# Kernel tuning notes

Hardware: AMD Instinct MI355X
Metric: run time of the kernel (lower is better)

The kernel has to match this reference:

```python
import jax, jax.numpy as jnp
import numpy as np

d_model = 512


def setup_inputs() -> dict:
    key = jax.random.key(0)
    k1, k2, k3, k4 = jax.random.split(key, 4)
    B, T, d_k = 8, 2048, 64
    scale = 1.0 / np.sqrt(d_model)
    x = jax.random.normal(k1, (B, T, d_model), dtype=jnp.float32)
    Wk = jax.random.normal(k2, (d_model, d_k), dtype=jnp.float32) * scale
    Wq = jax.random.normal(k3, (d_model, d_k), dtype=jnp.float32) * scale
    Wv = jax.random.normal(k4, (d_model, d_k), dtype=jnp.float32) * scale
    return {"x": x, "Wk": Wk, "Wq": Wq, "Wv": Wv}


def reference(x, Wk, Wq, Wv):
    # x: [B,T,C]; W*: [C,d_k]  (torch Linear weight is [d_k,C]; we store transposed)
    k = jnp.einsum('btc,cd->btd', x, Wk)
    q = jnp.einsum('btc,cd->btd', x, Wq)
    v = jnp.einsum('btc,cd->btd', x, Wv)
    d_k = k.shape[-1]
    scores = jnp.einsum('bqd,bkd->bqk', q, k) / jnp.sqrt(jnp.float32(d_k))
    attn = jax.nn.softmax(scores, axis=-1)  # [B,T,T]
    return jnp.einsum('bqk,bkd->bqd', attn, v)
```

## Files before the change

### kernel.cpp

```cpp
#include <hip/hip_runtime.h>
#include <hip/hip_bf16.h>
#include <stdint.h>


typedef short bf16x8 __attribute__((ext_vector_type(8)));
typedef float f32x4 __attribute__((ext_vector_type(4)));

#define MFMA_BF16 __builtin_amdgcn_mfma_f32_16x16x32_bf16

#define CEXP 0.18033688011112042f

__device__ __forceinline__ unsigned int pk2(float a, float b) {
    __hip_bfloat162 h = __float22bfloat162_rn(float2{a, b});
    union { __hip_bfloat162 h; unsigned int u; } r; r.h = h;
    return r.u;
}

__device__ __forceinline__ uint2 pack4_bf16(float a, float b, float c, float d) {
    uint2 r; r.x = pk2(a, b); r.y = pk2(c, d); return r;
}

__device__ __forceinline__ bf16x8 cvt8(f32x4 a, f32x4 b) {
    union { bf16x8 v; unsigned int u[4]; } r;
    r.u[0] = pk2(a[0], a[1]); r.u[1] = pk2(a[2], a[3]);
    r.u[2] = pk2(b[0], b[1]); r.u[3] = pk2(b[2], b[3]);
    return r.v;
}

__device__ __forceinline__ unsigned short bf1(float a) {
    __hip_bfloat16 h = __float2bfloat16(a);
    union { __hip_bfloat16 h; unsigned short u; } r; r.h = h;
    return r.u;
}

__global__ void wt_kernel(const float* __restrict__ Wq,
                          const float* __restrict__ Wk,
                          const float* __restrict__ Wv,
                          unsigned short* __restrict__ wt2)
{
    int id = blockIdx.x * 256 + threadIdx.x;
    int c    = id & 15;
    int quad = (id >> 4) & 3;
    int ks   = (id >> 6) & 15;
    int mt   = (id >> 10) & 3;
    int w    = id >> 12;
    const float* src = (w == 0) ? Wq : ((w == 1) ? Wk : Wv);
    const int n  = mt * 16 + c;
    const int k0 = ks * 32 + quad * 8;
    unsigned short* dst = wt2 + (size_t)id * 8;
    #pragma unroll
    for (int j = 0; j < 8; j++)
        dst[j] = bf1(src[(size_t)(k0 + j) * 64 + n]);
}

__global__ __launch_bounds__(256, 1) void proj_kernel(
    const float* __restrict__ x, const unsigned short* __restrict__ wt2,
    unsigned short* __restrict__ qg, unsigned short* __restrict__ kg2,
    unsigned short* __restrict__ vg2)
{
    __shared__ unsigned short xs[32768];

    const int tid  = threadIdx.x;
    const int lane = tid & 63;
    const int wave = tid >> 6;
    const int c    = lane & 15;
    const int quad = lane >> 4;
    const int tt   = blockIdx.x;
    const int t0   = tt * 64;

    const float* xb = x + (size_t)tt * 32768;
    #pragma unroll
    for (int t = 0; t < 16; t++) {
        int i = t * 256 + tid;
        f32x4 a = *(const f32x4*)(xb + (size_t)i * 8);
        f32x4 b = *(const f32x4*)(xb + (size_t)i * 8 + 4);
        int tok = i >> 6;
        int db  = i & 63;
        *(bf16x8*)(xs + ((size_t)db * 64 + (tok ^ (db & 7))) * 8) = cvt8(a, b);
    }
    __syncthreads();

    f32x4 acc[3][4];
    #pragma unroll
    for (int r = 0; r < 3; r++)
        #pragma unroll
        for (int st = 0; st < 4; st++) acc[r][st] = f32x4{0.f, 0.f, 0.f, 0.f};

    const int fbase = wave * 3;
    #pragma unroll 2
    for (int ks = 0; ks < 16; ks++) {
        bf16x8 wa[3];
        #pragma unroll
        for (int r = 0; r < 3; r++)
            wa[r] = *(const bf16x8*)(
                wt2 + ((size_t)((fbase + r) * 16 + ks) * 64 + lane) * 8);
        const int sw = c ^ ((ks & 1) * 4 + quad);
        const unsigned short* xrow = xs + ((size_t)(ks * 4 + quad) * 64 + sw) * 8;
        #pragma unroll
        for (int st = 0; st < 4; st++) {
            bf16x8 xf = *(const bf16x8*)(xrow + (size_t)st * 16 * 8);
            #pragma unroll
            for (int r = 0; r < 3; r++)
                acc[r][st] = MFMA_BF16(wa[r], xf, acc[r][st], 0, 0, 0);
        }
    }

    const int b = t0 >> 11;

    #pragma unroll
    for (int r = 0; r < 3; r++) {
        const int f  = fbase + r;
        const int w  = f >> 2;
        const int mt = f & 3;
        #pragma unroll
        for (int st = 0; st < 4; st++) {
            const int ts = t0 + st * 16;
            const int tb = ts & 2047;
            if (w == 0) {
                unsigned short* base = qg + (size_t)(ts + c) * 64;
                *(uint2*)(base + mt * 16 + quad * 4) =
                    pack4_bf16(acc[r][st][0] * CEXP, acc[r][st][1] * CEXP,
                               acc[r][st][2] * CEXP, acc[r][st][3] * CEXP);
            } else if (w == 1) {
                const int g  = tb >> 4;
                const int h  = mt >> 1;
                const int qk = (mt & 1) * 2 + (quad >> 1);
                size_t chunk = (size_t)b * 16384 + ((size_t)(g * 2 + h) * 4 + qk) * 16 + c;
                *(uint2*)(kg2 + chunk * 8 + (quad & 1) * 4) =
                    pack4_bf16(acc[r][st][0], acc[r][st][1], acc[r][st][2], acc[r][st][3]);
            } else {
                const int tk = tb + c;
                const int s  = tk >> 5;
                const int qv = (tk >> 3) & 3;
                const int j  = tk & 7;
                size_t chunk = (size_t)b * 16384 + ((size_t)(s * 4 + mt) * 4 + qv) * 16 + quad * 4;
                unsigned short* dst = vg2 + chunk * 8 + j;
                dst[0]  = bf1(acc[r][st][0]);
                dst[8]  = bf1(acc[r][st][1]);
                dst[16] = bf1(acc[r][st][2]);
                dst[24] = bf1(acc[r][st][3]);
            }
        }
    }
}

__global__ __launch_bounds__(512, 2) void attn_kernel(
    const unsigned short* __restrict__ qg, const unsigned short* __restrict__ kg2,
    const unsigned short* __restrict__ vg2, float* __restrict__ out)
{
    __shared__ __align__(16) unsigned short pt[8][4][16 * 136];
    __shared__ float lbuf[8][4][16];
    float* obase = reinterpret_cast<float*>(&pt[0][0][0]);

    const int lane = threadIdx.x & 63;
    const int wave = threadIdx.x >> 6;
    const int c    = lane & 15;
    const int quad = lane >> 4;
    const int b    = blockIdx.x & 7;
    const int g    = blockIdx.x >> 3;
    const int tb   = b * 2048 + g * 64;

    unsigned short* ptw = &pt[wave][0][0];
    const unsigned short* kbase = kg2 + ((size_t)b * 16384 + lane) * 8;
    const unsigned short* vbase = vg2 + ((size_t)b * 16384 + lane) * 8;

    bf16x8 qA0 = *(const bf16x8*)(qg + (size_t)(tb + c) * 64 + quad * 8);
    bf16x8 qA1 = *(const bf16x8*)(qg + (size_t)(tb + c) * 64 + 32 + quad * 8);
    bf16x8 qB0 = *(const bf16x8*)(qg + (size_t)(tb + 16 + c) * 64 + quad * 8);
    bf16x8 qB1 = *(const bf16x8*)(qg + (size_t)(tb + 16 + c) * 64 + 32 + quad * 8);
    bf16x8 qC0 = *(const bf16x8*)(qg + (size_t)(tb + 32 + c) * 64 + quad * 8);
    bf16x8 qC1 = *(const bf16x8*)(qg + (size_t)(tb + 32 + c) * 64 + 32 + quad * 8);
    bf16x8 qD0 = *(const bf16x8*)(qg + (size_t)(tb + 48 + c) * 64 + quad * 8);
    bf16x8 qD1 = *(const bf16x8*)(qg + (size_t)(tb + 48 + c) * 64 + 32 + quad * 8);

    bf16x8 ones;
    #pragma unroll
    for (int j = 0; j < 8; j++) ones[j] = (short)0x3F80;

    f32x4 oa0 = {0,0,0,0}, oa1 = {0,0,0,0}, oa2 = {0,0,0,0}, oa3 = {0,0,0,0};
    f32x4 ob0 = {0,0,0,0}, ob1 = {0,0,0,0}, ob2 = {0,0,0,0}, ob3 = {0,0,0,0};
    f32x4 oc0 = {0,0,0,0}, oc1 = {0,0,0,0}, oc2 = {0,0,0,0}, oc3 = {0,0,0,0};
    f32x4 od0 = {0,0,0,0}, od1 = {0,0,0,0}, od2 = {0,0,0,0}, od3 = {0,0,0,0};
    f32x4 laccA = {0,0,0,0}, laccB = {0,0,0,0};
    f32x4 laccC = {0,0,0,0}, laccD = {0,0,0,0};

    for (int kt = wave * 2; kt < wave * 2 + 2; kt++) {
        const int key0 = kt * 128;
        const int g0   = key0 >> 4;
        const int s0   = key0 >> 5;
        const f32x4 z = {0,0,0,0};

        bf16x8 va[2][4];
        #pragma unroll
        for (int mt = 0; mt < 4; mt++) {
            va[0][mt] = *(const bf16x8*)(vbase + (size_t)((s0    ) * 4 + mt) * 64 * 8);
            va[1][mt] = *(const bf16x8*)(vbase + (size_t)((s0 + 1) * 4 + mt) * 64 * 8);
        }

        #pragma unroll
        for (int mt = 0; mt < 8; mt++) {
            bf16x8 k0 = *(const bf16x8*)(kbase + (size_t)((g0 + mt) * 2    ) * 64 * 8);
            bf16x8 k1 = *(const bf16x8*)(kbase + (size_t)((g0 + mt) * 2 + 1) * 64 * 8);
            f32x4 sA = MFMA_BF16(k0, qA0, z, 0, 0, 0);
            sA = MFMA_BF16(k1, qA1, sA, 0, 0, 0);
            f32x4 sB = MFMA_BF16(k0, qB0, z, 0, 0, 0);
            sB = MFMA_BF16(k1, qB1, sB, 0, 0, 0);
            f32x4 sC = MFMA_BF16(k0, qC0, z, 0, 0, 0);
            sC = MFMA_BF16(k1, qC1, sC, 0, 0, 0);
            f32x4 sD = MFMA_BF16(k0, qD0, z, 0, 0, 0);
            sD = MFMA_BF16(k1, qD1, sD, 0, 0, 0);
            *(uint2*)(ptw            + c * 136 + mt * 16 + quad * 4) =
                pack4_bf16(__builtin_amdgcn_exp2f(sA[0]), __builtin_amdgcn_exp2f(sA[1]),
                           __builtin_amdgcn_exp2f(sA[2]), __builtin_amdgcn_exp2f(sA[3]));
            *(uint2*)(ptw +     2176 + c * 136 + mt * 16 + quad * 4) =
                pack4_bf16(__builtin_amdgcn_exp2f(sB[0]), __builtin_amdgcn_exp2f(sB[1]),
                           __builtin_amdgcn_exp2f(sB[2]), __builtin_amdgcn_exp2f(sB[3]));
            *(uint2*)(ptw + 2 * 2176 + c * 136 + mt * 16 + quad * 4) =
                pack4_bf16(__builtin_amdgcn_exp2f(sC[0]), __builtin_amdgcn_exp2f(sC[1]),
                           __builtin_amdgcn_exp2f(sC[2]), __builtin_amdgcn_exp2f(sC[3]));
            *(uint2*)(ptw + 3 * 2176 + c * 136 + mt * 16 + quad * 4) =
                pack4_bf16(__builtin_amdgcn_exp2f(sD[0]), __builtin_amdgcn_exp2f(sD[1]),
                           __builtin_amdgcn_exp2f(sD[2]), __builtin_amdgcn_exp2f(sD[3]));
        }
        asm volatile("" ::: "memory");

        #pragma unroll
        for (int ks = 0; ks < 4; ks++) {
            bf16x8 pbA = *(const bf16x8*)(ptw            + c * 136 + ks * 32 + quad * 8);
            bf16x8 pbB = *(const bf16x8*)(ptw +     2176 + c * 136 + ks * 32 + quad * 8);
            bf16x8 pbC = *(const bf16x8*)(ptw + 2 * 2176 + c * 136 + ks * 32 + quad * 8);
            bf16x8 pbD = *(const bf16x8*)(ptw + 3 * 2176 + c * 136 + ks * 32 + quad * 8);
            bf16x8 v0 = va[ks & 1][0], v1 = va[ks & 1][1];
            bf16x8 v2 = va[ks & 1][2], v3 = va[ks & 1][3];
            if (ks < 2) {
                #pragma unroll
                for (int mt = 0; mt < 4; mt++)
                    va[ks & 1][mt] =
                        *(const bf16x8*)(vbase + (size_t)((s0 + ks + 2) * 4 + mt) * 64 * 8);
            }
            oa0 = MFMA_BF16(v0, pbA, oa0, 0, 0, 0);
            oa1 = MFMA_BF16(v1, pbA, oa1, 0, 0, 0);
            oa2 = MFMA_BF16(v2, pbA, oa2, 0, 0, 0);
            oa3 = MFMA_BF16(v3, pbA, oa3, 0, 0, 0);
            laccA = MFMA_BF16(ones, pbA, laccA, 0, 0, 0);
            ob0 = MFMA_BF16(v0, pbB, ob0, 0, 0, 0);
            ob1 = MFMA_BF16(v1, pbB, ob1, 0, 0, 0);
            ob2 = MFMA_BF16(v2, pbB, ob2, 0, 0, 0);
            ob3 = MFMA_BF16(v3, pbB, ob3, 0, 0, 0);
            laccB = MFMA_BF16(ones, pbB, laccB, 0, 0, 0);
            oc0 = MFMA_BF16(v0, pbC, oc0, 0, 0, 0);
            oc1 = MFMA_BF16(v1, pbC, oc1, 0, 0, 0);
            oc2 = MFMA_BF16(v2, pbC, oc2, 0, 0, 0);
            oc3 = MFMA_BF16(v3, pbC, oc3, 0, 0, 0);
            laccC = MFMA_BF16(ones, pbC, laccC, 0, 0, 0);
            od0 = MFMA_BF16(v0, pbD, od0, 0, 0, 0);
            od1 = MFMA_BF16(v1, pbD, od1, 0, 0, 0);
            od2 = MFMA_BF16(v2, pbD, od2, 0, 0, 0);
            od3 = MFMA_BF16(v3, pbD, od3, 0, 0, 0);
            laccD = MFMA_BF16(ones, pbD, laccD, 0, 0, 0);
        }
        asm volatile("" ::: "memory");
    }

    if (quad == 0) {
        lbuf[wave][0][c] = laccA[0]; lbuf[wave][1][c] = laccB[0];
        lbuf[wave][2][c] = laccC[0]; lbuf[wave][3][c] = laccD[0];
    }

    __syncthreads();

    if (wave < 4) {
        float* o0 = obase + ((size_t)(wave * 4 + 0) * 16 + c) * 68 + quad * 4;
        float* o1 = obase + ((size_t)(wave * 4 + 1) * 16 + c) * 68 + quad * 4;
        float* o2 = obase + ((size_t)(wave * 4 + 2) * 16 + c) * 68 + quad * 4;
        float* o3 = obase + ((size_t)(wave * 4 + 3) * 16 + c) * 68 + quad * 4;
        *(f32x4*)(o0 +  0) = oa0; *(f32x4*)(o0 + 16) = oa1;
        *(f32x4*)(o0 + 32) = oa2; *(f32x4*)(o0 + 48) = oa3;
        *(f32x4*)(o1 +  0) = ob0; *(f32x4*)(o1 + 16) = ob1;
        *(f32x4*)(o1 + 32) = ob2; *(f32x4*)(o1 + 48) = ob3;
        *(f32x4*)(o2 +  0) = oc0; *(f32x4*)(o2 + 16) = oc1;
        *(f32x4*)(o2 + 32) = oc2; *(f32x4*)(o2 + 48) = oc3;
        *(f32x4*)(o3 +  0) = od0; *(f32x4*)(o3 + 16) = od1;
        *(f32x4*)(o3 + 32) = od2; *(f32x4*)(o3 + 48) = od3;
    }
    __syncthreads();

    if (wave >= 4) {
        const int p = wave - 4;
        float* o0 = obase + ((size_t)(p * 4 + 0) * 16 + c) * 68 + quad * 4;
        float* o1 = obase + ((size_t)(p * 4 + 1) * 16 + c) * 68 + quad * 4;
        float* o2 = obase + ((size_t)(p * 4 + 2) * 16 + c) * 68 + quad * 4;
        float* o3 = obase + ((size_t)(p * 4 + 3) * 16 + c) * 68 + quad * 4;
        #define ADDSTORE(ptr, off, reg) { f32x4 t = *(f32x4*)((ptr) + (off)); \
            t[0] += reg[0]; t[1] += reg[1]; t[2] += reg[2]; t[3] += reg[3];   \
            *(f32x4*)((ptr) + (off)) = t; }
        ADDSTORE(o0,  0, oa0); ADDSTORE(o0, 16, oa1);
        ADDSTORE(o0, 32, oa2); ADDSTORE(o0, 48, oa3);
        ADDSTORE(o1,  0, ob0); ADDSTORE(o1, 16, ob1);
        ADDSTORE(o1, 32, ob2); ADDSTORE(o1, 48, ob3);
        ADDSTORE(o2,  0, oc0); ADDSTORE(o2, 16, oc1);
        ADDSTORE(o2, 32, oc2); ADDSTORE(o2, 48, oc3);
        ADDSTORE(o3,  0, od0); ADDSTORE(o3, 16, od1);
        ADDSTORE(o3, 32, od2); ADDSTORE(o3, 48, od3);
        #undef ADDSTORE
    }
    __syncthreads();

    const int tid = threadIdx.x;
    const int row = tid >> 3;
    const int d0  = (tid & 7) * 8;
    const int qt  = row >> 4;
    const int r   = row & 15;
    float L = 0.f;
    #pragma unroll
    for (int w = 0; w < 8; w++) L += lbuf[w][qt][r];
    const float rl = 1.f / L;
    f32x4 Oa = {0,0,0,0}, Ob = {0,0,0,0};
    #pragma unroll
    for (int p = 0; p < 4; p++) {
        const float* src = obase + ((size_t)(p * 4 + qt) * 16 + r) * 68 + d0;
        f32x4 a   = *(const f32x4*)(src);
        f32x4 bfr = *(const f32x4*)(src + 4);
        Oa[0] += a[0]; Oa[1] += a[1]; Oa[2] += a[2]; Oa[3] += a[3];
        Ob[0] += bfr[0]; Ob[1] += bfr[1]; Ob[2] += bfr[2]; Ob[3] += bfr[3];
    }
    Oa[0] *= rl; Oa[1] *= rl; Oa[2] *= rl; Oa[3] *= rl;
    Ob[0] *= rl; Ob[1] *= rl; Ob[2] *= rl; Ob[3] *= rl;
    float* op = out + (size_t)(tb + row) * 64 + d0;
    *(f32x4*)op       = Oa;
    *(f32x4*)(op + 4) = Ob;
}

extern "C" void kernel_launch(void* const* d_in, const int* in_sizes, int n_in,
                              void* d_out, int out_size, void* d_ws, size_t ws_size,
                              hipStream_t stream)
{
    const float* x  = (const float*)d_in[0];
    const float* Wk = (const float*)d_in[1];
    const float* Wq = (const float*)d_in[2];
    const float* Wv = (const float*)d_in[3];
    float* out = (float*)d_out;

    char* ws = (char*)d_ws;
    unsigned short* qg  = (unsigned short*)(ws);
    unsigned short* kg2 = (unsigned short*)(ws + (2u << 20));
    unsigned short* vg2 = (unsigned short*)(ws + (4u << 20));
    unsigned short* wt2 = (unsigned short*)(ws + (6u << 20));

    hipLaunchKernelGGL(wt_kernel,   dim3(48),   dim3(256), 0, stream,
                       Wq, Wk, Wv, wt2);
    hipLaunchKernelGGL(proj_kernel, dim3(256),  dim3(256), 0, stream,
                       x, wt2, qg, kg2, vg2);
    hipLaunchKernelGGL(attn_kernel, dim3(256),  dim3(512), 0, stream,
                       qg, kg2, vg2, out);
}
```

Before: 102.3 us.

## Fuse weight prep, projection and attention into one cooperative kernel

Merges the weight transpose/convert kernel, the QKV projection kernel and the attention kernel into a single cooperative launch. Grid-wide syncs separate the stages, and one shared-memory buffer is reused for the x tile, the P tiles and the output reduction. This removes two kernel launches and the gaps between them. In exchange it adds two grid barriers, uses only 4 of 8 waves during projection, and caps occupancy at one large-LDS block per CU.

```diff
diff --git a/kernel.cpp b/kernel.cpp
--- a/kernel.cpp
+++ b/kernel.cpp
@@ -1,7 +1,10 @@
 #include <hip/hip_runtime.h>
+#include <hip/hip_cooperative_groups.h>
 #include <hip/hip_bf16.h>
 #include <stdint.h>
 
+
+namespace cg = cooperative_groups;
 
 typedef short bf16x8 __attribute__((ext_vector_type(8)));
 typedef float f32x4 __attribute__((ext_vector_type(4)));
@@ -33,134 +36,135 @@
     return r.u;
 }
 
-__global__ void wt_kernel(const float* __restrict__ Wq,
-                          const float* __restrict__ Wk,
-                          const float* __restrict__ Wv,
-                          unsigned short* __restrict__ wt2)
+__global__ __launch_bounds__(512, 2) void fused_kernel(
+    const float* __restrict__ x,
+    const float* __restrict__ Wq, const float* __restrict__ Wk,
+    const float* __restrict__ Wv,
+    unsigned short* __restrict__ qg, unsigned short* __restrict__ kg2,
+    unsigned short* __restrict__ vg2, unsigned short* __restrict__ wt2,
+    float* __restrict__ out)
 {
-    int id = blockIdx.x * 256 + threadIdx.x;
-    int c    = id & 15;
-    int quad = (id >> 4) & 3;
-    int ks   = (id >> 6) & 15;
-    int mt   = (id >> 10) & 3;
-    int w    = id >> 12;
-    const float* src = (w == 0) ? Wq : ((w == 1) ? Wk : Wv);
-    const int n  = mt * 16 + c;
-    const int k0 = ks * 32 + quad * 8;
-    unsigned short* dst = wt2 + (size_t)id * 8;
-    #pragma unroll
-    for (int j = 0; j < 8; j++)
-        dst[j] = bf1(src[(size_t)(k0 + j) * 64 + n]);
-}
-
-__global__ __launch_bounds__(256, 1) void proj_kernel(
-    const float* __restrict__ x, const unsigned short* __restrict__ wt2,
-    unsigned short* __restrict__ qg, unsigned short* __restrict__ kg2,
-    unsigned short* __restrict__ vg2)
-{
-    __shared__ unsigned short xs[32768];
+    __shared__ __align__(16) unsigned char smem[141312];
+
+    cg::grid_group grid = cg::this_grid();
 
     const int tid  = threadIdx.x;
+    const int bid  = blockIdx.x;
     const int lane = tid & 63;
     const int wave = tid >> 6;
     const int c    = lane & 15;
     const int quad = lane >> 4;
-    const int tt   = blockIdx.x;
-    const int t0   = tt * 64;
-
-    const float* xb = x + (size_t)tt * 32768;
-    #pragma unroll
-    for (int t = 0; t < 16; t++) {
-        int i = t * 256 + tid;
-        f32x4 a = *(const f32x4*)(xb + (size_t)i * 8);
-        f32x4 b = *(const f32x4*)(xb + (size_t)i * 8 + 4);
-        int tok = i >> 6;
-        int db  = i & 63;
-        *(bf16x8*)(xs + ((size_t)db * 64 + (tok ^ (db & 7))) * 8) = cvt8(a, b);
-    }
-    __syncthreads();
-
-    f32x4 acc[3][4];
-    #pragma unroll
-    for (int r = 0; r < 3; r++)
-        #pragma unroll
-        for (int st = 0; st < 4; st++) acc[r][st] = f32x4{0.f, 0.f, 0.f, 0.f};
-
-    const int fbase = wave * 3;
-    #pragma unroll 2
-    for (int ks = 0; ks < 16; ks++) {
-        bf16x8 wa[3];
+
+    if ((tid & 7) == 0 && tid < 384) {
+        int id = bid * 48 + (tid >> 3);
+        int cw   = id & 15;
+        int qw   = (id >> 4) & 3;
+        int ksw  = (id >> 6) & 15;
+        int mtw  = (id >> 10) & 3;
+        int w    = id >> 12;
+        const float* src = (w == 0) ? Wq : ((w == 1) ? Wk : Wv);
+        const int n  = mtw * 16 + cw;
+        const int k0 = ksw * 32 + qw * 8;
+        unsigned short* dst = wt2 + (size_t)id * 8;
+        #pragma unroll
+        for (int j = 0; j < 8; j++)
+            dst[j] = bf1(src[(size_t)(k0 + j) * 64 + n]);
+    }
+
+    {
+        unsigned short* xs = (unsigned short*)smem;
+        const float* xb = x + (size_t)bid * 32768;
+        #pragma unroll
+        for (int t = 0; t < 8; t++) {
+            int i = t * 512 + tid;
+            f32x4 a = *(const f32x4*)(xb + (size_t)i * 8);
+            f32x4 b = *(const f32x4*)(xb + (size_t)i * 8 + 4);
+            int tok = i >> 6;
+            int db  = i & 63;
+            *(bf16x8*)(xs + ((size_t)db * 64 + (tok ^ (db & 7))) * 8) = cvt8(a, b);
+        }
+    }
+
+    grid.sync();
+
+    if (wave < 4) {
+        const unsigned short* xs = (const unsigned short*)smem;
+        const int t0 = bid * 64;
+
+        f32x4 acc[3][4];
         #pragma unroll
         for (int r = 0; r < 3; r++)
-            wa[r] = *(const bf16x8*)(
-                wt2 + ((size_t)((fbase + r) * 16 + ks) * 64 + lane) * 8);
-        const int sw = c ^ ((ks & 1) * 4 + quad);
-        const unsigned short* xrow = xs + ((size_t)(ks * 4 + quad) * 64 + sw) * 8;
-        #pragma unroll
-        for (int st = 0; st < 4; st++) {
-            bf16x8 xf = *(const bf16x8*)(xrow + (size_t)st * 16 * 8);
+            #pragma unroll
+            for (int st = 0; st < 4; st++) acc[r][st] = f32x4{0.f, 0.f, 0.f, 0.f};
+
+        const int fbase = wave * 3;
+        #pragma unroll 2
+        for (int ks = 0; ks < 16; ks++) {
+            bf16x8 wa[3];
             #pragma unroll
             for (int r = 0; r < 3; r++)
-                acc[r][st] = MFMA_BF16(wa[r], xf, acc[r][st], 0, 0, 0);
-        }
-    }
-
-    const int b = t0 >> 11;
-
-    #pragma unroll
-    for (int r = 0; r < 3; r++) {
-        const int f  = fbase + r;
-        const int w  = f >> 2;
-        const int mt = f & 3;
-        #pragma unroll
-        for (int st = 0; st < 4; st++) {
-            const int ts = t0 + st * 16;
-            const int tb = ts & 2047;
-            if (w == 0) {
-                unsigned short* base = qg + (size_t)(ts + c) * 64;
-                *(uint2*)(base + mt * 16 + quad * 4) =
-                    pack4_bf16(acc[r][st][0] * CEXP, acc[r][st][1] * CEXP,
-                               acc[r][st][2] * CEXP, acc[r][st][3] * CEXP);
-            } else if (w == 1) {
-                const int g  = tb >> 4;
-                const int h  = mt >> 1;
-                const int qk = (mt & 1) * 2 + (quad >> 1);
-                size_t chunk = (size_t)b * 16384 + ((size_t)(g * 2 + h) * 4 + qk) * 16 + c;
-                *(uint2*)(kg2 + chunk * 8 + (quad & 1) * 4) =
-                    pack4_bf16(acc[r][st][0], acc[r][st][1], acc[r][st][2], acc[r][st][3]);
-            } else {
-                const int tk = tb + c;
-                const int s  = tk >> 5;
-                const int qv = (tk >> 3) & 3;
-                const int j  = tk & 7;
-                size_t chunk = (size_t)b * 16384 + ((size_t)(s * 4 + mt) * 4 + qv) * 16 + quad * 4;
-                unsigned short* dst = vg2 + chunk * 8 + j;
-                dst[0]  = bf1(acc[r][st][0]);
-                dst[8]  = bf1(acc[r][st][1]);
-                dst[16] = bf1(acc[r][st][2]);
-                dst[24] = bf1(acc[r][st][3]);
+                wa[r] = *(const bf16x8*)(
+                    wt2 + ((size_t)((fbase + r) * 16 + ks) * 64 + lane) * 8);
+            const int sw = c ^ ((ks & 1) * 4 + quad);
+            const unsigned short* xrow = xs + ((size_t)(ks * 4 + quad) * 64 + sw) * 8;
+            #pragma unroll
+            for (int st = 0; st < 4; st++) {
+                bf16x8 xf = *(const bf16x8*)(xrow + (size_t)st * 16 * 8);
+                #pragma unroll
+                for (int r = 0; r < 3; r++)
+                    acc[r][st] = MFMA_BF16(wa[r], xf, acc[r][st], 0, 0, 0);
             }
         }
-    }
-}
-
-__global__ __launch_bounds__(512, 2) void attn_kernel(
-    const unsigned short* __restrict__ qg, const unsigned short* __restrict__ kg2,
-    const unsigned short* __restrict__ vg2, float* __restrict__ out)
-{
-    __shared__ __align__(16) unsigned short pt[8][4][16 * 136];
-    __shared__ float lbuf[8][4][16];
-    float* obase = reinterpret_cast<float*>(&pt[0][0][0]);
-
-    const int lane = threadIdx.x & 63;
-    const int wave = threadIdx.x >> 6;
-    const int c    = lane & 15;
-    const int quad = lane >> 4;
-    const int b    = blockIdx.x & 7;
-    const int g    = blockIdx.x >> 3;
-    const int tb   = b * 2048 + g * 64;
-
-    unsigned short* ptw = &pt[wave][0][0];
+
+        const int b = t0 >> 11;
+        #pragma unroll
+        for (int r = 0; r < 3; r++) {
+            const int f  = fbase + r;
+            const int w  = f >> 2;
+            const int mt = f & 3;
+            #pragma unroll
+            for (int st = 0; st < 4; st++) {
+                const int ts = t0 + st * 16;
+                const int tb = ts & 2047;
+                if (w == 0) {
+                    unsigned short* base = qg + (size_t)(ts + c) * 64;
+                    *(uint2*)(base + mt * 16 + quad * 4) =
+                        pack4_bf16(acc[r][st][0] * CEXP, acc[r][st][1] * CEXP,
+                                   acc[r][st][2] * CEXP, acc[r][st][3] * CEXP);
+                } else if (w == 1) {
+                    const int g  = tb >> 4;
+                    const int h  = mt >> 1;
+                    const int qk = (mt & 1) * 2 + (quad >> 1);
+                    size_t chunk = (size_t)b * 16384 + ((size_t)(g * 2 + h) * 4 + qk) * 16 + c;
+                    *(uint2*)(kg2 + chunk * 8 + (quad & 1) * 4) =
+                        pack4_bf16(acc[r][st][0], acc[r][st][1], acc[r][st][2], acc[r][st][3]);
+                } else {
+                    const int tk = tb + c;
+                    const int s  = tk >> 5;
+                    const int qv = (tk >> 3) & 3;
+                    const int j  = tk & 7;
+                    size_t chunk = (size_t)b * 16384 + ((size_t)(s * 4 + mt) * 4 + qv) * 16 + quad * 4;
+                    unsigned short* dst = vg2 + chunk * 8 + j;
+                    dst[0]  = bf1(acc[r][st][0]);
+                    dst[8]  = bf1(acc[r][st][1]);
+                    dst[16] = bf1(acc[r][st][2]);
+                    dst[24] = bf1(acc[r][st][3]);
+                }
+            }
+        }
+    }
+
+    grid.sync();
+
+    unsigned short* ptall = (unsigned short*)smem;
+    float* lbuf  = (float*)(smem + 139264);
+    float* obase = (float*)smem;
+
+    const int b  = bid & 7;
+    const int g  = bid >> 3;
+    const int tb = b * 2048 + g * 64;
+
+    unsigned short* ptw = ptall + (size_t)wave * 4 * 2176;
     const unsigned short* kbase = kg2 + ((size_t)b * 16384 + lane) * 8;
     const unsigned short* vbase = vg2 + ((size_t)b * 16384 + lane) * 8;
 
@@ -263,8 +267,10 @@
     }
 
     if (quad == 0) {
-        lbuf[wave][0][c] = laccA[0]; lbuf[wave][1][c] = laccB[0];
-        lbuf[wave][2][c] = laccC[0]; lbuf[wave][3][c] = laccD[0];
+        lbuf[(wave * 4 + 0) * 16 + c] = laccA[0];
+        lbuf[(wave * 4 + 1) * 16 + c] = laccB[0];
+        lbuf[(wave * 4 + 2) * 16 + c] = laccC[0];
+        lbuf[(wave * 4 + 3) * 16 + c] = laccD[0];
     }
 
     __syncthreads();
@@ -306,14 +312,13 @@
     }
     __syncthreads();
 
-    const int tid = threadIdx.x;
     const int row = tid >> 3;
     const int d0  = (tid & 7) * 8;
     const int qt  = row >> 4;
     const int r   = row & 15;
     float L = 0.f;
     #pragma unroll
-    for (int w = 0; w < 8; w++) L += lbuf[w][qt][r];
+    for (int w = 0; w < 8; w++) L += lbuf[(w * 4 + qt) * 16 + r];
     const float rl = 1.f / L;
     f32x4 Oa = {0,0,0,0}, Ob = {0,0,0,0};
     #pragma unroll
@@ -347,10 +352,9 @@
     unsigned short* vg2 = (unsigned short*)(ws + (4u << 20));
     unsigned short* wt2 = (unsigned short*)(ws + (6u << 20));
 
-    hipLaunchKernelGGL(wt_kernel,   dim3(48),   dim3(256), 0, stream,
-                       Wq, Wk, Wv, wt2);
-    hipLaunchKernelGGL(proj_kernel, dim3(256),  dim3(256), 0, stream,
-                       x, wt2, qg, kg2, vg2);
-    hipLaunchKernelGGL(attn_kernel, dim3(256),  dim3(512), 0, stream,
-                       qg, kg2, vg2, out);
-}
+    void* args[9] = { (void*)&x, (void*)&Wq, (void*)&Wk, (void*)&Wv,
+                      (void*)&qg, (void*)&kg2, (void*)&vg2, (void*)&wt2,
+                      (void*)&out };
+    hipLaunchCooperativeKernel((const void*)fused_kernel, dim3(256), dim3(512),
+                               args, 0, stream);
+}
```

After: 172.0 us. +68.1%, slower.
